# Performance work log

Measured on AMD Instinct MI355X. Metric: run time of the kernel, lower is better.

Reference implementation:

```python
import jax, jax.numpy as jnp
import numpy as np


def setup_inputs() -> dict:
    key = jax.random.key(0)
    k1, k2, k3 = jax.random.split(key, 3)
    T, B, C, H, W = 64, 2, 32, 32, 32
    x_seq = jax.random.normal(k1, (T, B, C, H, W), dtype=jnp.float32)
    A_kernel = jax.random.normal(k2, (C, 3, 3), dtype=jnp.float32) * 0.1
    B_kernel = jax.random.normal(k3, (C, 3, 3), dtype=jnp.float32) * 0.1
    return {"x_seq": x_seq, "A_kernel": A_kernel, "B_kernel": B_kernel}


def reference(x_seq, A_kernel, B_kernel):
    # ConvSSM recurrence h_t = A * h_{t-1} + B * x_t (circular conv via zero-padded FFT)
    # computed with an associative parallel scan in the frequency domain.
    H, W = x_seq.shape[-2], x_seq.shape[-1]
    fft_size = (2 * H, 2 * W)
    axes = (-2, -1)

    x_f = jnp.fft.rfftn(x_seq.astype(jnp.float32), s=fft_size, axes=axes)  # (T,B,C,2H,W+1) complex
    A_f = jnp.fft.rfftn(A_kernel.astype(jnp.float32), s=fft_size, axes=axes)  # (C,2H,W+1)
    B_f = jnpp_rfft = jnp.fft.rfftn(B_kernel.astype(jnp.float32), s=fft_size, axes=axes)

    # scan elements: (a_t, s_t) with a_t = A_f, s_t = B_f * X_t
    a = jnp.broadcast_to(A_f[None, None], x_f.shape)
    s = x_f * B_f[None, None]

    def combine(left, right):
        # (a1,s1) (+) (a2,s2) = (a1*a2, s1*a2 + s2); left is earlier in time
        a1, s1 = left
        a2, s2 = right
        return (a1 * a2, s1 * a2 + s2)

    _, h_f = jax.lax.associative_scan(combine, (a, s), axis=0)

    h = jnp.fft.irfftn(h_f, s=fft_size, axes=axes)  # (T,B,C,2H,2W) real
    return h[..., :H, :W].astype(x_seq.dtype)
```

## Files before the change

### kernel.cpp

```cpp
#include <hip/hip_runtime.h>


constexpr int T_STEPS = 64;
constexpr int B_DIM   = 2;
constexpr int C_DIM   = 32;
constexpr int HW      = 32;
constexpr int N       = 64;
constexpr int NIMG    = B_DIM * C_DIM;
constexpr int MH      = T_STEPS / 2;
constexpr int HSTR    = 68;
constexpr int GSZ     = 36 * 36;
constexpr int USZ     = HW * HW;

__device__ __forceinline__ float rfl(float v) {
    return __int_as_float(__builtin_amdgcn_readfirstlane(__float_as_int(v)));
}

__device__ __forceinline__ float ror1(float x) {
    return __int_as_float(__builtin_amdgcn_update_dpp(
        0, __float_as_int(x), 0x121, 0xF, 0xF, false));
}

__global__ __launch_bounds__(256)
void convssm_pass1d(const float* __restrict__ x_seq,
                    const float* __restrict__ A_k,
                    const float* __restrict__ B_k,
                    float* __restrict__ U,
                    float* __restrict__ G)
{
    __shared__ __align__(16) float xe[32][36];
    __shared__ __align__(16) float xo[32][36];
    __shared__ __align__(16) float ue[34][36];

    const int blk = blockIdx.x;
    const int m   = blk >> 6;
    const int bc  = blk & 63;
    const int c   = bc & 31;
    const int tid = threadIdx.x;

    float a[9], bw[9];
#pragma unroll
    for (int i = 0; i < 9; ++i) { a[i] = A_k[c * 9 + i]; bw[i] = B_k[c * 9 + i]; }

    const float4* xE = (const float4*)(x_seq + ((size_t)(2 * m)     * NIMG + bc) * (HW * HW));
    const float4* xO = (const float4*)(x_seq + ((size_t)(2 * m + 1) * NIMG + bc) * (HW * HW));
    {
        const int y  = tid >> 3;
        const int x4 = (tid & 7) * 4;
        *(float4*)&xe[y][x4] = xE[tid];
        *(float4*)&xo[y][x4] = xO[tid];
    }
    __syncthreads();

    for (int i = tid; i < 34 * 34; i += 256) {
        int y = i / 34, xx = i - y * 34;
        float v = 0.0f;
#pragma unroll
        for (int ky = 0; ky < 3; ++ky) {
            int yy = y - ky;
            if (yy < 0 || yy >= 32) continue;
#pragma unroll
            for (int kx = 0; kx < 3; ++kx) {
                int xs = xx - kx;
                if (xs < 0 || xs >= 32) continue;
                v += bw[ky * 3 + kx] * xe[yy][xs];
            }
        }
        ue[y][xx] = v;
    }
    __syncthreads();

    float* Ug = U + (size_t)(bc * MH + m) * USZ;
    {
        const int y  = tid >> 3;
        const int x4 = (tid & 7) * 4;
        *(float4*)(Ug + y * HW + x4) = *(const float4*)&ue[y][x4];
    }

    float* Gg = G + (size_t)(bc * MH + m) * GSZ;
    for (int i4 = tid; i4 < 324; i4 += 256) {
        const int y  = i4 / 9;
        const int x0 = (i4 - y * 9) * 4;
        float r[4];
#pragma unroll
        for (int j = 0; j < 4; ++j) {
            const int xx = x0 + j;
            float v = 0.0f;
#pragma unroll
            for (int ky = 0; ky < 3; ++ky) {
#pragma unroll
                for (int kx = 0; kx < 3; ++kx) {
                    int yy = y - ky, xs = xx - kx;
                    if (yy >= 0 && yy < 32 && xs >= 0 && xs < 32)
                        v += bw[ky * 3 + kx] * xo[yy][xs];
                    if (yy >= 0 && yy < 34 && xs >= 0 && xs < 34)
                        v += a[ky * 3 + kx] * ue[yy][xs];
                }
            }
            r[j] = v;
        }
        *(float4*)(Gg + y * 36 + x0) = make_float4(r[0], r[1], r[2], r[3]);
    }
}

__global__ __launch_bounds__(1024)
void convssm_scan6(const float* __restrict__ U,
                   const float* __restrict__ G,
                   const float* __restrict__ A_k,
                   float* __restrict__ out)
{
    __shared__ __align__(16) float hbuf[2][N * HSTR];

    const int bc  = blockIdx.x;
    const int c   = bc & 31;
    const int tid = threadIdx.x;
    const int g   = tid & 15;
    const int y   = tid >> 4;
    const int xc  = g * 4;

    float af[9];
#pragma unroll
    for (int i = 0; i < 9; ++i) af[i] = A_k[c * 9 + i];

    float a2f[25];
#pragma unroll
    for (int p = 0; p < 5; ++p) {
#pragma unroll
        for (int q = 0; q < 5; ++q) {
            float v = 0.0f;
#pragma unroll
            for (int ky = 0; ky < 3; ++ky) {
                int py = p - ky;
                if (py < 0 || py > 2) continue;
#pragma unroll
                for (int kx = 0; kx < 3; ++kx) {
                    int qx = q - kx;
                    if (qx < 0 || qx > 2) continue;
                    v += af[ky * 3 + kx] * af[py * 3 + qx];
                }
            }
            a2f[p * 5 + q] = v;
        }
    }
#pragma unroll
    for (int i = 0; i < 25; ++i) a2f[i] = rfl(a2f[i]);
#pragma unroll
    for (int i = 0; i < 9; ++i)  af[i]  = rfl(af[i]);

    for (int i = tid; i < N * HSTR; i += 1024) hbuf[0][i] = 0.0f;

    const bool cropw = (y < HW);
    const bool crop  = cropw && (xc < HW);
    const bool gok   = (y < 36) && (xc <= 32);

    const float* Ub = U + (size_t)bc * MH * USZ + y * HW + xc;
    const float* Gb = G + (size_t)bc * MH * GSZ + y * 36 + xc;

    const float4 z4 = make_float4(0.f, 0.f, 0.f, 0.f);
    float4 gc = z4, uc = z4;
    if (gok)  gc = *(const float4*)(Gb);
    if (crop) uc = *(const float4*)(Ub);

    float* hold = &hbuf[0][0];
    float* hnew = &hbuf[1][0];
    float* ob   = out + (size_t)bc * (HW * HW);
    const size_t tstr = (size_t)NIMG * (HW * HW);

    float4 acc = z4;

    __syncthreads();

    for (int m = 0; m < MH; ++m) {
        float4 gn = z4, un = z4;
        if (m + 1 < MH) {
            if (gok)  gn = *(const float4*)(Gb + (size_t)(m + 1) * GSZ);
            if (crop) un = *(const float4*)(Ub + (size_t)(m + 1) * USZ);
        }

        float4 hi[4];
#pragma unroll
        for (int i = 0; i < 4; ++i) {
            const int rr = (y + 60 + i) & 63;
            hi[i] = *(const float4*)(hold + rr * HSTR + xc);
        }

        float w[5][8];
#pragma unroll
        for (int i = 0; i < 4; ++i) {
            w[i][4] = hi[i].x; w[i][5] = hi[i].y; w[i][6] = hi[i].z; w[i][7] = hi[i].w;
            w[i][0] = ror1(hi[i].x); w[i][1] = ror1(hi[i].y);
            w[i][2] = ror1(hi[i].z); w[i][3] = ror1(hi[i].w);
        }
        w[4][4] = acc.x; w[4][5] = acc.y; w[4][6] = acc.z; w[4][7] = acc.w;
        w[4][0] = ror1(acc.x); w[4][1] = ror1(acc.y);
        w[4][2] = ror1(acc.z); w[4][3] = ror1(acc.w);

        float o[4] = { gc.x, gc.y, gc.z, gc.w };
#pragma unroll
        for (int p = 0; p < 5; ++p) {
            const int i = 4 - p;
#pragma unroll
            for (int q = 0; q < 5; ++q) {
                const float cf = a2f[p * 5 + q];
#pragma unroll
                for (int j = 0; j < 4; ++j)
                    o[j] += cf * w[i][4 + j - q];
            }
        }
        const float4 accn = make_float4(o[0], o[1], o[2], o[3]);

        if (cropw) {
            float e[4] = { uc.x, uc.y, uc.z, uc.w };
#pragma unroll
            for (int ky = 0; ky < 3; ++ky) {
                const int i = 4 - ky;
#pragma unroll
                for (int kx = 0; kx < 3; ++kx) {
                    const float cf = af[ky * 3 + kx];
#pragma unroll
                    for (int j = 0; j < 4; ++j)
                        e[j] += cf * w[i][4 + j - kx];
                }
            }
            if (crop) {
                float* oe = ob + (size_t)(2 * m) * tstr;
                *(float4*)(oe + y * HW + xc) = make_float4(e[0], e[1], e[2], e[3]);
                *(float4*)(oe + tstr + y * HW + xc) = accn;
            }
        }

        *(float4*)(hnew + y * HSTR + xc) = accn;

        __syncthreads();

        float* tmp = hold; hold = hnew; hnew = tmp;
        acc = accn;
        gc = gn; uc = un;
    }
}

__global__ __launch_bounds__(256)
void convssm_scan_fused(const float* __restrict__ x_seq,
                        const float* __restrict__ A_k,
                        const float* __restrict__ B_k,
                        float* __restrict__ out)
{
    __shared__ float h0[N][N];
    __shared__ float h1[N][N];
    __shared__ float xs[N][N];

    const int bc = blockIdx.x;
    const int b  = bc >> 5;
    const int c  = bc & 31;
    const int tid = threadIdx.x;
    const int x   = tid & 63;
    const int y0  = (tid >> 6) << 4;

    float a[9], bw[9];
#pragma unroll
    for (int i = 0; i < 9; ++i) { a[i] = A_k[c*9+i]; bw[i] = B_k[c*9+i]; }
#pragma unroll
    for (int r = 0; r < 16; ++r) { h0[y0+r][x] = 0.f; xs[y0+r][x] = 0.f; }

    float (*hold)[N] = h0;
    float (*hnew)[N] = h1;
    const int xm1 = (x + 63) & 63, xm2 = (x + 62) & 63;
    const size_t img = (size_t)HW*HW, tstr = (size_t)NIMG*img;
    const float* xbase = x_seq + ((size_t)b*C_DIM + c)*img;
    float* obase = out + ((size_t)b*C_DIM + c)*img;
    const bool loader = (x < HW);

    for (int t = 0; t < T_STEPS; ++t) {
        if (loader) {
#pragma unroll
            for (int r = 0; r < 16; ++r) {
                int yy = y0 + r;
                if (yy < HW) xs[yy][x] = xbase[(size_t)t*tstr + yy*HW + x];
            }
        }
        __syncthreads();
        const int ym1 = (y0 + N - 1) & 63, ym2 = (y0 + N - 2) & 63;
        float hr1c0 = hold[ym1][x], hr1c1 = hold[ym1][xm1], hr1c2 = hold[ym1][xm2];
        float hr2c0 = hold[ym2][x], hr2c1 = hold[ym2][xm1], hr2c2 = hold[ym2][xm2];
        float sr1c0 = xs[ym1][x], sr1c1 = xs[ym1][xm1], sr1c2 = xs[ym1][xm2];
        float sr2c0 = xs[ym2][x], sr2c1 = xs[ym2][xm1], sr2c2 = xs[ym2][xm2];
#pragma unroll
        for (int r = 0; r < 16; ++r) {
            const int yy = y0 + r;
            float hr0c0 = hold[yy][x], hr0c1 = hold[yy][xm1], hr0c2 = hold[yy][xm2];
            float sr0c0 = xs[yy][x], sr0c1 = xs[yy][xm1], sr0c2 = xs[yy][xm2];
            float v = a[0]*hr0c0 + a[1]*hr0c1 + a[2]*hr0c2
                    + a[3]*hr1c0 + a[4]*hr1c1 + a[5]*hr1c2
                    + a[6]*hr2c0 + a[7]*hr2c1 + a[8]*hr2c2
                    + bw[0]*sr0c0 + bw[1]*sr0c1 + bw[2]*sr0c2
                    + bw[3]*sr1c0 + bw[4]*sr1c1 + bw[5]*sr1c2
                    + bw[6]*sr2c0 + bw[7]*sr2c1 + bw[8]*sr2c2;
            hnew[yy][x] = v;
            if (yy < HW && x < HW) obase[(size_t)t*tstr + yy*HW + x] = v;
            hr2c0=hr1c0; hr2c1=hr1c1; hr2c2=hr1c2;
            hr1c0=hr0c0; hr1c1=hr0c1; hr1c2=hr0c2;
            sr2c0=sr1c0; sr2c1=sr1c1; sr2c2=sr1c2;
            sr1c0=sr0c0; sr1c1=sr0c1; sr1c2=sr0c2;
        }
        __syncthreads();
        float (*tmp)[N] = hold; hold = hnew; hnew = tmp;
    }
}

extern "C" void kernel_launch(void* const* d_in, const int* in_sizes, int n_in,
                              void* d_out, int out_size, void* d_ws, size_t ws_size,
                              hipStream_t stream)
{
    const float* x_seq = (const float*)d_in[0];
    const float* A_k   = (const float*)d_in[1];
    const float* B_k   = (const float*)d_in[2];
    float* out = (float*)d_out;

    const size_t needU = (size_t)NIMG * MH * USZ;
    const size_t needG = (size_t)NIMG * MH * GSZ;
    const size_t need  = (needU + needG) * sizeof(float);

    if (ws_size >= need) {
        float* U = (float*)d_ws;
        float* G = U + needU;
        convssm_pass1d<<<dim3(MH * NIMG), dim3(256), 0, stream>>>(
            x_seq, A_k, B_k, U, G);
        convssm_scan6<<<dim3(NIMG), dim3(1024), 0, stream>>>(
            U, G, A_k, out);
    } else {
        convssm_scan_fused<<<dim3(NIMG), dim3(256), 0, stream>>>(
            x_seq, A_k, B_k, out);
    }
}
```

Before: 64.63 us.

## Switch to stride-4 recurrence with A^4 kernel and separate emit pass

Replaces the stride-2 scan (A^2 over 32 steps) with a stride-4 scan using the 9x9 A^4 kernel over 16 serial steps. A parallel pre-pass builds the cascaded 4-step input contributions and the A^2/A^3/A^4 coefficients. A new parallel emit kernel reconstructs the three intermediate timesteps from the saved cropped states. This halves the serial sequential steps in the latency-bound scan, at the cost of a larger stencil per step, an extra kernel launch and more workspace traffic.

```diff
diff --git a/kernel.cpp b/kernel.cpp
--- a/kernel.cpp
+++ b/kernel.cpp
@@ -7,30 +7,79 @@
 constexpr int HW      = 32;
 constexpr int N       = 64;
 constexpr int NIMG    = B_DIM * C_DIM;
-constexpr int MH      = T_STEPS / 2;
+constexpr int MQ      = 16;
 constexpr int HSTR    = 68;
-constexpr int GSZ     = 36 * 36;
-constexpr int USZ     = HW * HW;
+constexpr int G4ROW   = 40;
+constexpr int G4SZT   = 40 * 40;
+constexpr int SROWS   = 40;
+constexpr int SSZT    = SROWS * 64;
+constexpr int CO_A2 = 0, CO_A3 = 25, CO_A4 = 74, CO_STRIDE = 160;
 
 __device__ __forceinline__ float rfl(float v) {
     return __int_as_float(__builtin_amdgcn_readfirstlane(__float_as_int(v)));
 }
-
 __device__ __forceinline__ float ror1(float x) {
     return __int_as_float(__builtin_amdgcn_update_dpp(
         0, __float_as_int(x), 0x121, 0xF, 0xF, false));
 }
 
+__device__ __forceinline__ void cascade_stage(
+    float* __restrict__ dst, const float* __restrict__ src, int SI, int SO,
+    const float (*xsf)[36], const float* a9, const float* bw9,
+    int tid, int nthr)
+{
+    const int niter = SO * 10;
+    for (int i4 = tid; i4 < niter; i4 += nthr) {
+        const int y  = i4 / 10;
+        const int x0 = (i4 - y * 10) * 4;
+        float r[4] = {0.f, 0.f, 0.f, 0.f};
+#pragma unroll
+        for (int ky = 0; ky < 3; ++ky) {
+            const int yy = y - ky;
+            if (yy >= 0 && yy < 32) {
+                float xr[6];
+#pragma unroll
+                for (int d = 0; d < 6; ++d) {
+                    const int xq = x0 - 2 + d;
+                    xr[d] = (xq >= 0 && xq < 32) ? xsf[yy][xq] : 0.f;
+                }
+#pragma unroll
+                for (int kx = 0; kx < 3; ++kx) {
+                    const float cf = bw9[ky * 3 + kx];
+#pragma unroll
+                    for (int j = 0; j < 4; ++j) r[j] += cf * xr[2 + j - kx];
+                }
+            }
+            if (SI > 0 && yy >= 0 && yy < SI) {
+                float sr[6];
+#pragma unroll
+                for (int d = 0; d < 6; ++d) {
+                    const int xq = x0 - 2 + d;
+                    sr[d] = (xq >= 0 && xq < SI) ? src[yy * 40 + xq] : 0.f;
+                }
+#pragma unroll
+                for (int kx = 0; kx < 3; ++kx) {
+                    const float cf = a9[ky * 3 + kx];
+#pragma unroll
+                    for (int j = 0; j < 4; ++j) r[j] += cf * sr[2 + j - kx];
+                }
+            }
+        }
+        *(float4*)(dst + y * 40 + x0) = make_float4(r[0], r[1], r[2], r[3]);
+    }
+}
+
 __global__ __launch_bounds__(256)
-void convssm_pass1d(const float* __restrict__ x_seq,
+void convssm_pass1q(const float* __restrict__ x_seq,
                     const float* __restrict__ A_k,
                     const float* __restrict__ B_k,
-                    float* __restrict__ U,
-                    float* __restrict__ G)
-{
-    __shared__ __align__(16) float xe[32][36];
-    __shared__ __align__(16) float xo[32][36];
-    __shared__ __align__(16) float ue[34][36];
+                    float* __restrict__ G4,
+                    float* __restrict__ coef)
+{
+    __shared__ __align__(16) float xs[4][32][36];
+    __shared__ __align__(16) float bufA[38 * 40];
+    __shared__ __align__(16) float bufB[36 * 40];
+    __shared__ float a2l[25];
 
     const int blk = blockIdx.x;
     const int m   = blk >> 6;
@@ -38,76 +87,86 @@
     const int c   = bc & 31;
     const int tid = threadIdx.x;
 
+    float* Gg = G4 + (size_t)(bc * (MQ + 1) + m) * G4SZT;
+    const float4 z4 = make_float4(0.f, 0.f, 0.f, 0.f);
+
+    if (m == MQ) {
+        for (int i4 = tid; i4 < 400; i4 += 256)
+            *(float4*)(Gg + i4 * 4) = z4;
+        return;
+    }
+
     float a[9], bw[9];
 #pragma unroll
-    for (int i = 0; i < 9; ++i) { a[i] = A_k[c * 9 + i]; bw[i] = B_k[c * 9 + i]; }
-
-    const float4* xE = (const float4*)(x_seq + ((size_t)(2 * m)     * NIMG + bc) * (HW * HW));
-    const float4* xO = (const float4*)(x_seq + ((size_t)(2 * m + 1) * NIMG + bc) * (HW * HW));
+    for (int i = 0; i < 9; ++i) {
+        a[i]  = rfl(A_k[c * 9 + i]);
+        bw[i] = rfl(B_k[c * 9 + i]);
+    }
+
     {
         const int y  = tid >> 3;
         const int x4 = (tid & 7) * 4;
-        *(float4*)&xe[y][x4] = xE[tid];
-        *(float4*)&xo[y][x4] = xO[tid];
-    }
-    __syncthreads();
-
-    for (int i = tid; i < 34 * 34; i += 256) {
-        int y = i / 34, xx = i - y * 34;
-        float v = 0.0f;
-#pragma unroll
-        for (int ky = 0; ky < 3; ++ky) {
-            int yy = y - ky;
-            if (yy < 0 || yy >= 32) continue;
-#pragma unroll
-            for (int kx = 0; kx < 3; ++kx) {
-                int xs = xx - kx;
-                if (xs < 0 || xs >= 32) continue;
-                v += bw[ky * 3 + kx] * xe[yy][xs];
-            }
-        }
-        ue[y][xx] = v;
-    }
-    __syncthreads();
-
-    float* Ug = U + (size_t)(bc * MH + m) * USZ;
-    {
-        const int y  = tid >> 3;
-        const int x4 = (tid & 7) * 4;
-        *(float4*)(Ug + y * HW + x4) = *(const float4*)&ue[y][x4];
-    }
-
-    float* Gg = G + (size_t)(bc * MH + m) * GSZ;
-    for (int i4 = tid; i4 < 324; i4 += 256) {
-        const int y  = i4 / 9;
-        const int x0 = (i4 - y * 9) * 4;
-        float r[4];
-#pragma unroll
-        for (int j = 0; j < 4; ++j) {
-            const int xx = x0 + j;
-            float v = 0.0f;
-#pragma unroll
-            for (int ky = 0; ky < 3; ++ky) {
-#pragma unroll
+#pragma unroll
+        for (int f = 0; f < 4; ++f) {
+            const float* xp = x_seq + ((size_t)(4 * m + f) * NIMG + bc) * (HW * HW);
+            *(float4*)&xs[f][y][x4] = *(const float4*)(xp + y * HW + x4);
+        }
+    }
+    __syncthreads();
+
+    cascade_stage(bufA, nullptr, 0, 34, xs[0], a, bw, tid, 256);
+    __syncthreads();
+    cascade_stage(bufB, bufA, 34, 36, xs[1], a, bw, tid, 256);
+    __syncthreads();
+    cascade_stage(bufA, bufB, 36, 38, xs[2], a, bw, tid, 256);
+    __syncthreads();
+    cascade_stage(Gg,   bufA, 38, 40, xs[3], a, bw, tid, 256);
+
+    if (m == 0 && bc < 32) {
+        __syncthreads();
+        if (tid < 25) {
+            const int p = tid / 5, q = tid - (tid / 5) * 5;
+            float v = 0.f;
+            for (int ky = 0; ky < 3; ++ky)
                 for (int kx = 0; kx < 3; ++kx) {
-                    int yy = y - ky, xs = xx - kx;
-                    if (yy >= 0 && yy < 32 && xs >= 0 && xs < 32)
-                        v += bw[ky * 3 + kx] * xo[yy][xs];
-                    if (yy >= 0 && yy < 34 && xs >= 0 && xs < 34)
-                        v += a[ky * 3 + kx] * ue[yy][xs];
-                }
-            }
-            r[j] = v;
-        }
-        *(float4*)(Gg + y * 36 + x0) = make_float4(r[0], r[1], r[2], r[3]);
-    }
-}
-
-__global__ __launch_bounds__(1024)
-void convssm_scan6(const float* __restrict__ U,
-                   const float* __restrict__ G,
-                   const float* __restrict__ A_k,
-                   float* __restrict__ out)
+                    const int py = p - ky, qx = q - kx;
+                    if (py >= 0 && py < 3 && qx >= 0 && qx < 3)
+                        v += a[ky * 3 + kx] * a[py * 3 + qx];
+                }
+            a2l[tid] = v;
+            coef[c * CO_STRIDE + CO_A2 + tid] = v;
+        }
+        __syncthreads();
+        if (tid < 49) {
+            const int p = tid / 7, q = tid - (tid / 7) * 7;
+            float v = 0.f;
+            for (int i = 0; i < 5; ++i)
+                for (int j = 0; j < 5; ++j) {
+                    const int py = p - i, qx = q - j;
+                    if (py >= 0 && py < 3 && qx >= 0 && qx < 3)
+                        v += a2l[i * 5 + j] * a[py * 3 + qx];
+                }
+            coef[c * CO_STRIDE + CO_A3 + tid] = v;
+        }
+        if (tid >= 64 && tid < 145) {
+            const int t = tid - 64;
+            const int p = t / 9, q = t - (t / 9) * 9;
+            float v = 0.f;
+            for (int i = 0; i < 5; ++i)
+                for (int j = 0; j < 5; ++j) {
+                    const int py = p - i, qx = q - j;
+                    if (py >= 0 && py < 5 && qx >= 0 && qx < 5)
+                        v += a2l[i * 5 + j] * a2l[py * 5 + qx];
+                }
+            coef[c * CO_STRIDE + CO_A4 + t] = v;
+        }
+    }
+}
+
+__global__ __launch_bounds__(512, 2)
+void convssm_scanq(const float* __restrict__ G4,
+                   const float* __restrict__ coef,
+                   float* __restrict__ S)
 {
     __shared__ __align__(16) float hbuf[2][N * HSTR];
 
@@ -115,128 +174,218 @@
     const int c   = bc & 31;
     const int tid = threadIdx.x;
     const int g   = tid & 15;
-    const int y   = tid >> 4;
+    const int s   = tid >> 4;
+    const int y0  = s * 2;
     const int xc  = g * 4;
 
-    float af[9];
-#pragma unroll
-    for (int i = 0; i < 9; ++i) af[i] = A_k[c * 9 + i];
-
-    float a2f[25];
-#pragma unroll
-    for (int p = 0; p < 5; ++p) {
-#pragma unroll
-        for (int q = 0; q < 5; ++q) {
-            float v = 0.0f;
-#pragma unroll
-            for (int ky = 0; ky < 3; ++ky) {
-                int py = p - ky;
-                if (py < 0 || py > 2) continue;
-#pragma unroll
-                for (int kx = 0; kx < 3; ++kx) {
-                    int qx = q - kx;
-                    if (qx < 0 || qx > 2) continue;
-                    v += af[ky * 3 + kx] * af[py * 3 + qx];
-                }
-            }
-            a2f[p * 5 + q] = v;
-        }
-    }
-#pragma unroll
-    for (int i = 0; i < 25; ++i) a2f[i] = rfl(a2f[i]);
-#pragma unroll
-    for (int i = 0; i < 9; ++i)  af[i]  = rfl(af[i]);
-
-    for (int i = tid; i < N * HSTR; i += 1024) hbuf[0][i] = 0.0f;
-
-    const bool cropw = (y < HW);
-    const bool crop  = cropw && (xc < HW);
-    const bool gok   = (y < 36) && (xc <= 32);
-
-    const float* Ub = U + (size_t)bc * MH * USZ + y * HW + xc;
-    const float* Gb = G + (size_t)bc * MH * GSZ + y * 36 + xc;
+    float a4[81];
+    {
+        const float* cb = coef + c * CO_STRIDE + CO_A4;
+#pragma unroll
+        for (int i = 0; i < 81; ++i) a4[i] = rfl(cb[i]);
+    }
+
+    for (int i = tid; i < N * HSTR; i += 512) hbuf[0][i] = 0.0f;
+
+    const bool  gok = (y0 < G4ROW) && (xc < G4ROW);
+    const float* Gb = G4 + (size_t)bc * (MQ + 1) * G4SZT + y0 * G4ROW + xc;
 
     const float4 z4 = make_float4(0.f, 0.f, 0.f, 0.f);
-    float4 gc = z4, uc = z4;
-    if (gok)  gc = *(const float4*)(Gb);
-    if (crop) uc = *(const float4*)(Ub);
+    float4 gc0 = z4, gc1 = z4;
+    if (gok) {
+        gc0 = *(const float4*)(Gb);
+        gc1 = *(const float4*)(Gb + G4ROW);
+    }
 
     float* hold = &hbuf[0][0];
     float* hnew = &hbuf[1][0];
-    float* ob   = out + (size_t)bc * (HW * HW);
+    float* Sb   = S + (size_t)bc * MQ * SSZT;
+    const bool sok  = (y0 < 32) || (y0 >= 56);
+    const int  slot = (y0 < 32) ? y0 : (y0 - 24);
+
+    float4 acc0 = z4, acc1 = z4;
+
+    __syncthreads();
+
+    for (int m = 0; m < MQ; ++m) {
+        float4 gn0 = z4, gn1 = z4;
+        if (gok) {
+            const float* p = Gb + (size_t)(m + 1) * G4SZT;
+            gn0 = *(const float4*)(p);
+            gn1 = *(const float4*)(p + G4ROW);
+        }
+
+        float o0[4] = {gc0.x, gc0.y, gc0.z, gc0.w};
+        float o1[4] = {gc1.x, gc1.y, gc1.z, gc1.w};
+
+#pragma unroll
+        for (int i = 0; i < 10; ++i) {
+            float4 d4;
+            if (i < 8) {
+                const int rr = (y0 + 56 + i) & 63;
+                d4 = *(const float4*)(hold + rr * HSTR + xc);
+            } else {
+                d4 = (i == 8) ? acc0 : acc1;
+            }
+            float w[12];
+            w[8] = d4.x; w[9] = d4.y; w[10] = d4.z; w[11] = d4.w;
+            w[4] = ror1(d4.x); w[5] = ror1(d4.y); w[6] = ror1(d4.z); w[7] = ror1(d4.w);
+            w[0] = ror1(w[4]); w[1] = ror1(w[5]); w[2] = ror1(w[6]); w[3] = ror1(w[7]);
+
+            if (i <= 8) {
+                const int p = 8 - i;
+#pragma unroll
+                for (int q = 0; q < 9; ++q) {
+                    const float cf = a4[p * 9 + q];
+#pragma unroll
+                    for (int j = 0; j < 4; ++j) o0[j] += cf * w[8 + j - q];
+                }
+            }
+            if (i >= 1) {
+                const int p = 9 - i;
+#pragma unroll
+                for (int q = 0; q < 9; ++q) {
+                    const float cf = a4[p * 9 + q];
+#pragma unroll
+                    for (int j = 0; j < 4; ++j) o1[j] += cf * w[8 + j - q];
+                }
+            }
+        }
+        const float4 accn0 = make_float4(o0[0], o0[1], o0[2], o0[3]);
+        const float4 accn1 = make_float4(o1[0], o1[1], o1[2], o1[3]);
+
+        *(float4*)(hnew + y0 * HSTR + xc)       = accn0;
+        *(float4*)(hnew + (y0 + 1) * HSTR + xc) = accn1;
+        if (sok) {
+            float* sp = Sb + (size_t)m * SSZT + slot * 64 + xc;
+            *(float4*)(sp)      = accn0;
+            *(float4*)(sp + 64) = accn1;
+        }
+
+        __syncthreads();
+
+        float* t = hold; hold = hnew; hnew = t;
+        acc0 = accn0; acc1 = accn1;
+        gc0 = gn0; gc1 = gn1;
+    }
+}
+
+__global__ __launch_bounds__(256)
+void convssm_emitq(const float* __restrict__ x_seq,
+                   const float* __restrict__ A_k,
+                   const float* __restrict__ B_k,
+                   const float* __restrict__ coef,
+                   const float* __restrict__ S,
+                   float* __restrict__ out)
+{
+    __shared__ __align__(16) float Sl[SROWS][68];
+    __shared__ __align__(16) float xs[3][32][36];
+    __shared__ __align__(16) float c0b[34 * 40];
+    __shared__ __align__(16) float c1b[36 * 40];
+    __shared__ __align__(16) float c2b[38 * 40];
+    __shared__ float cl[96];
+
+    const int blk = blockIdx.x;
+    const int m   = blk >> 6;
+    const int bc  = blk & 63;
+    const int c   = bc & 31;
+    const int tid = threadIdx.x;
+
+    float a[9], bw[9];
+#pragma unroll
+    for (int i = 0; i < 9; ++i) {
+        a[i]  = rfl(A_k[c * 9 + i]);
+        bw[i] = rfl(B_k[c * 9 + i]);
+    }
+    if (tid < 74) cl[tid] = coef[c * CO_STRIDE + tid];
+
+    {
+        const int y  = tid >> 3;
+        const int x4 = (tid & 7) * 4;
+#pragma unroll
+        for (int f = 0; f < 3; ++f) {
+            const float* xp = x_seq + ((size_t)(4 * m + f) * NIMG + bc) * (HW * HW);
+            *(float4*)&xs[f][y][x4] = *(const float4*)(xp + y * HW + x4);
+        }
+    }
+    if (m > 0) {
+        const float* Sp = S + (size_t)(bc * MQ + (m - 1)) * SSZT;
+        for (int i4 = tid; i4 < 640; i4 += 256) {
+            const int y  = i4 >> 4;
+            const int x4 = (i4 & 15) * 4;
+            *(float4*)&Sl[y][x4] = *(const float4*)(Sp + y * 64 + x4);
+        }
+    }
+    __syncthreads();
+
+    cascade_stage(c0b, nullptr, 0, 34, xs[0], a, bw, tid, 256);
+    __syncthreads();
+    cascade_stage(c1b, c0b, 34, 36, xs[1], a, bw, tid, 256);
+    __syncthreads();
+    cascade_stage(c2b, c1b, 36, 38, xs[2], a, bw, tid, 256);
+    __syncthreads();
+
+    const int y  = tid >> 3;
+    const int x0 = (tid & 7) * 4;
+
+    float4 i0 = *(const float4*)(c0b + y * 40 + x0);
+    float4 i1 = *(const float4*)(c1b + y * 40 + x0);
+    float4 i2 = *(const float4*)(c2b + y * 40 + x0);
+    float e0[4] = {i0.x, i0.y, i0.z, i0.w};
+    float e1[4] = {i1.x, i1.y, i1.z, i1.w};
+    float e2[4] = {i2.x, i2.y, i2.z, i2.w};
+
+    if (m > 0) {
+        const int xm8 = (x0 + 56) & 63;
+        const int xm4 = (x0 + 60) & 63;
+#pragma unroll
+        for (int i = 0; i < 7; ++i) {
+            const int rr   = (y + 58 + i) & 63;
+            const int slot = (rr < 32) ? rr : (rr - 24);
+            const float4 l4 = *(const float4*)(&Sl[slot][xm8]);
+            const float4 m4 = *(const float4*)(&Sl[slot][xm4]);
+            const float4 d4 = *(const float4*)(&Sl[slot][x0]);
+            float w[12] = {l4.x, l4.y, l4.z, l4.w,
+                           m4.x, m4.y, m4.z, m4.w,
+                           d4.x, d4.y, d4.z, d4.w};
+            {
+                const int p = 6 - i;
+#pragma unroll
+                for (int q = 0; q < 7; ++q) {
+                    const float cf = cl[CO_A3 + p * 7 + q];
+#pragma unroll
+                    for (int j = 0; j < 4; ++j) e2[j] += cf * w[8 + j - q];
+                }
+            }
+            if (i >= 2) {
+                const int p = 6 - i;
+#pragma unroll
+                for (int q = 0; q < 5; ++q) {
+                    const float cf = cl[CO_A2 + p * 5 + q];
+#pragma unroll
+                    for (int j = 0; j < 4; ++j) e1[j] += cf * w[8 + j - q];
+                }
+            }
+            if (i >= 4) {
+                const int p = 6 - i;
+#pragma unroll
+                for (int q = 0; q < 3; ++q) {
+                    const float cf = a[p * 3 + q];
+#pragma unroll
+                    for (int j = 0; j < 4; ++j) e0[j] += cf * w[8 + j - q];
+                }
+            }
+        }
+    }
+
+    const float4 e3 = *(const float4*)(S + (size_t)(bc * MQ + m) * SSZT + y * 64 + x0);
+
     const size_t tstr = (size_t)NIMG * (HW * HW);
-
-    float4 acc = z4;
-
-    __syncthreads();
-
-    for (int m = 0; m < MH; ++m) {
-        float4 gn = z4, un = z4;
-        if (m + 1 < MH) {
-            if (gok)  gn = *(const float4*)(Gb + (size_t)(m + 1) * GSZ);
-            if (crop) un = *(const float4*)(Ub + (size_t)(m + 1) * USZ);
-        }
-
-        float4 hi[4];
-#pragma unroll
-        for (int i = 0; i < 4; ++i) {
-            const int rr = (y + 60 + i) & 63;
-            hi[i] = *(const float4*)(hold + rr * HSTR + xc);
-        }
-
-        float w[5][8];
-#pragma unroll
-        for (int i = 0; i < 4; ++i) {
-            w[i][4] = hi[i].x; w[i][5] = hi[i].y; w[i][6] = hi[i].z; w[i][7] = hi[i].w;
-            w[i][0] = ror1(hi[i].x); w[i][1] = ror1(hi[i].y);
-            w[i][2] = ror1(hi[i].z); w[i][3] = ror1(hi[i].w);
-        }
-        w[4][4] = acc.x; w[4][5] = acc.y; w[4][6] = acc.z; w[4][7] = acc.w;
-        w[4][0] = ror1(acc.x); w[4][1] = ror1(acc.y);
-        w[4][2] = ror1(acc.z); w[4][3] = ror1(acc.w);
-
-        float o[4] = { gc.x, gc.y, gc.z, gc.w };
-#pragma unroll
-        for (int p = 0; p < 5; ++p) {
-            const int i = 4 - p;
-#pragma unroll
-            for (int q = 0; q < 5; ++q) {
-                const float cf = a2f[p * 5 + q];
-#pragma unroll
-                for (int j = 0; j < 4; ++j)
-                    o[j] += cf * w[i][4 + j - q];
-            }
-        }
-        const float4 accn = make_float4(o[0], o[1], o[2], o[3]);
-
-        if (cropw) {
-            float e[4] = { uc.x, uc.y, uc.z, uc.w };
-#pragma unroll
-            for (int ky = 0; ky < 3; ++ky) {
-                const int i = 4 - ky;
-#pragma unroll
-                for (int kx = 0; kx < 3; ++kx) {
-                    const float cf = af[ky * 3 + kx];
-#pragma unroll
-                    for (int j = 0; j < 4; ++j)
-                        e[j] += cf * w[i][4 + j - kx];
-                }
-            }
-            if (crop) {
-                float* oe = ob + (size_t)(2 * m) * tstr;
-                *(float4*)(oe + y * HW + xc) = make_float4(e[0], e[1], e[2], e[3]);
-                *(float4*)(oe + tstr + y * HW + xc) = accn;
-            }
-        }
-
-        *(float4*)(hnew + y * HSTR + xc) = accn;
-
-        __syncthreads();
-
-        float* tmp = hold; hold = hnew; hnew = tmp;
-        acc = accn;
-        gc = gn; uc = un;
-    }
+    float* ob = out + (size_t)(4 * m) * tstr + (size_t)bc * (HW * HW) + y * HW + x0;
+    *(float4*)(ob)            = make_float4(e0[0], e0[1], e0[2], e0[3]);
+    *(float4*)(ob + tstr)     = make_float4(e1[0], e1[1], e1[2], e1[3]);
+    *(float4*)(ob + 2 * tstr) = make_float4(e2[0], e2[1], e2[2], e2[3]);
+    *(float4*)(ob + 3 * tstr) = e3;
 }
 
 __global__ __launch_bounds__(256)
@@ -247,7 +396,7 @@
 {
     __shared__ float h0[N][N];
     __shared__ float h1[N][N];
-    __shared__ float xs[N][N];
+    __shared__ float xsf[N][N];
 
     const int bc = blockIdx.x;
     const int b  = bc >> 5;
@@ -260,7 +409,7 @@
 #pragma unroll
     for (int i = 0; i < 9; ++i) { a[i] = A_k[c*9+i]; bw[i] = B_k[c*9+i]; }
 #pragma unroll
-    for (int r = 0; r < 16; ++r) { h0[y0+r][x] = 0.f; xs[y0+r][x] = 0.f; }
+    for (int r = 0; r < 16; ++r) { h0[y0+r][x] = 0.f; xsf[y0+r][x] = 0.f; }
 
     float (*hold)[N] = h0;
     float (*hnew)[N] = h1;
@@ -275,20 +424,20 @@
 #pragma unroll
             for (int r = 0; r < 16; ++r) {
                 int yy = y0 + r;
-                if (yy < HW) xs[yy][x] = xbase[(size_t)t*tstr + yy*HW + x];
+                if (yy < HW) xsf[yy][x] = xbase[(size_t)t*tstr + yy*HW + x];
             }
         }
         __syncthreads();
         const int ym1 = (y0 + N - 1) & 63, ym2 = (y0 + N - 2) & 63;
         float hr1c0 = hold[ym1][x], hr1c1 = hold[ym1][xm1], hr1c2 = hold[ym1][xm2];
         float hr2c0 = hold[ym2][x], hr2c1 = hold[ym2][xm1], hr2c2 = hold[ym2][xm2];
-        float sr1c0 = xs[ym1][x], sr1c1 = xs[ym1][xm1], sr1c2 = xs[ym1][xm2];
-        float sr2c0 = xs[ym2][x], sr2c1 = xs[ym2][xm1], sr2c2 = xs[ym2][xm2];
+        float sr1c0 = xsf[ym1][x], sr1c1 = xsf[ym1][xm1], sr1c2 = xsf[ym1][xm2];
+        float sr2c0 = xsf[ym2][x], sr2c1 = xsf[ym2][xm1], sr2c2 = xsf[ym2][xm2];
 #pragma unroll
         for (int r = 0; r < 16; ++r) {
             const int yy = y0 + r;
             float hr0c0 = hold[yy][x], hr0c1 = hold[yy][xm1], hr0c2 = hold[yy][xm2];
-            float sr0c0 = xs[yy][x], sr0c1 = xs[yy][xm1], sr0c2 = xs[yy][xm2];
+            float sr0c0 = xsf[yy][x], sr0c1 = xsf[yy][xm1], sr0c2 = xsf[yy][xm2];
             float v = a[0]*hr0c0 + a[1]*hr0c1 + a[2]*hr0c2
                     + a[3]*hr1c0 + a[4]*hr1c1 + a[5]*hr1c2
                     + a[6]*hr2c0 + a[7]*hr2c1 + a[8]*hr2c2
@@ -316,17 +465,20 @@
     const float* B_k   = (const float*)d_in[2];
     float* out = (float*)d_out;
 
-    const size_t needU = (size_t)NIMG * MH * USZ;
-    const size_t needG = (size_t)NIMG * MH * GSZ;
-    const size_t need  = (needU + needG) * sizeof(float);
+    const size_t nG4 = (size_t)NIMG * (MQ + 1) * G4SZT;
+    const size_t nCF = 32 * CO_STRIDE;
+    const size_t nS  = (size_t)NIMG * MQ * SSZT;
+    const size_t need = (nG4 + nCF + nS) * sizeof(float);
 
     if (ws_size >= need) {
-        float* U = (float*)d_ws;
-        float* G = U + needU;
-        convssm_pass1d<<<dim3(MH * NIMG), dim3(256), 0, stream>>>(
-            x_seq, A_k, B_k, U, G);
-        convssm_scan6<<<dim3(NIMG), dim3(1024), 0, stream>>>(
-            U, G, A_k, out);
+        float* G4c = (float*)d_ws;
+        float* cf  = G4c + nG4;
+        float* Sg  = cf + nCF;
+        convssm_pass1q<<<dim3((MQ + 1) * NIMG), dim3(256), 0, stream>>>(
+            x_seq, A_k, B_k, G4c, cf);
+        convssm_scanq<<<dim3(NIMG), dim3(512), 0, stream>>>(G4c, cf, Sg);
+        convssm_emitq<<<dim3(MQ * NIMG), dim3(256), 0, stream>>>(
+            x_seq, A_k, B_k, cf, Sg, out);
     } else {
         convssm_scan_fused<<<dim3(NIMG), dim3(256), 0, stream>>>(
             x_seq, A_k, B_k, out);
```

After: 95.84 us. 1.48x slower.
